# Performance work log

Measured on AMD Instinct MI355X. Metric: run time of the kernel, lower is better.

## Reference

```python
import jax, jax.numpy as jnp
import numpy as np

IN_CHANNELS = 192
KERNEL_SIZE = 3
GROUPS = 1
N_ITER = 3  # power_it_niter


def _gram_conv(K):
    """Gram step of the conv operator: G[a, b] = sum_o corr(K[o, a], K[o, b]).

    K: (co, ci, k, k) -> (ci, ci, 2k-1, 2k-1). This is the kernel of M^T M
    where M is the (zero-padded) conv operator with kernel K.
    """
    k = K.shape[-1]
    lhs = jnp.transpose(K, (1, 0, 2, 3))  # batch = a-index, channels = o
    rhs = jnp.transpose(K, (1, 0, 2, 3))  # out-chan = b-index, in-chan = o
    return jax.lax.conv_general_dilated(
        lhs, rhs, window_strides=(1, 1),
        padding=[(k - 1, k - 1), (k - 1, k - 1)],
        dimension_numbers=("NCHW", "OIHW", "NCHW"))


def _sigma_one_group(K, n_iter):
    """Gram-iteration spectral-norm estimate (Delattre et al. 2024).

    sigma(K_0) ~= prod_t f_t^(1/2^t) * ||K_T||_F^(1/2^T), f_t = Frobenius norm
    before each Gram squaring (normalization keeps values in fp range).
    """
    log_sigma = jnp.asarray(0.0, K.dtype)
    for t in range(n_iter):  # static unroll: kernel spatial size grows k -> 2k-1
        f = jnp.sqrt(jnp.sum(K * K))
        K = K / f
        log_sigma = log_sigma + jnp.log(f) / (2.0 ** t)
        K = _gram_conv(K)
    f_final = jnp.sqrt(jnp.sum(K * K))
    log_sigma = log_sigma + jnp.log(f_final) / (2.0 ** n_iter)
    return jnp.exp(log_sigma)


def compute_delattre2024(K, n_iter):
    # K: (groups, c, c, k, k) -> (groups,) per-group spectral norm estimates
    return jax.vmap(lambda g: _sigma_one_group(g, n_iter))(K)


def setup_inputs() -> dict:
    key = jax.random.key(0)
    kernel = jax.random.normal(
        key, (IN_CHANNELS * GROUPS, IN_CHANNELS, KERNEL_SIZE, KERNEL_SIZE),
        dtype=jnp.float32)
    return {"kernel": kernel}


def reference(kernel):
    g = GROUPS
    c = IN_CHANNELS // GROUPS
    K = kernel.reshape(g, c, c, KERNEL_SIZE, KERNEL_SIZE)
    sigmas = compute_delattre2024(K, N_ITER)  # (groups,)
    K = K / sigmas.reshape(-1, 1, 1, 1, 1)
    return K.reshape(IN_CHANNELS * GROUPS, IN_CHANNELS, KERNEL_SIZE, KERNEL_SIZE)
```

## Files before the change

### kernel.cpp

```cpp
#include <hip/hip_runtime.h>
#include <hip/hip_bf16.h>

typedef __bf16 bf16;
typedef __attribute__((ext_vector_type(8))) __bf16 bf16x8;
typedef __attribute__((ext_vector_type(4))) __bf16 bf16x4;
typedef __attribute__((ext_vector_type(4))) float f32x4;
typedef __attribute__((ext_vector_type(4))) int i32x4;
typedef __attribute__((ext_vector_type(2))) int i32x2;

#define CH 192
#define MAT (CH * CH)
#define NF 145
#define NELEM (CH * CH * 9)
#define XSCALE 9.765625e-4f
#define W17 0.36959913571644626f


__device__ __forceinline__ int swz8(int c, int r) {
    return (c & ~7) | ((c & 7) ^ (r & 7));
}

__global__ void k_tr(const float* __restrict__ K, float* __restrict__ Kt,
                     float* __restrict__ s3) {
    int p = blockIdx.x * 256 + threadIdx.x;
    if (p == 0) *s3 = 0.0f;
    int o = p / CH, a = p % CH;
    const float* src = K + (size_t)p * 9;
#pragma unroll
    for (int i = 0; i < 9; ++i)
        Kt[(size_t)i * MAT + a * CH + o] = src[i];
}

__global__ __launch_bounds__(1024, 4)
__attribute__((amdgpu_waves_per_eu(4, 4)))
void k_g3(const float* __restrict__ Kt, float* __restrict__ s3) {
    __shared__ __align__(16) bf16 lds[2 * MAT];
    __shared__ float twc[17], tws[17];
    __shared__ float red[16];
    int f = blockIdx.x;
    int tid = threadIdx.x;
    int lane = tid & 63, w = tid >> 6;
    int ml = lane & 15, kqc = lane >> 4;
    int rb = (w >> 2) * 48;
    int cb = (w & 3) * 48;

    if (tid < 17) {
        float s, c;
        __sincosf(-W17 * (float)tid, &s, &c);
        twc[tid] = c; tws[tid] = s;
    }
    __syncthreads();

    int fy, fx;
    if (f < 9) { fy = 0; fx = f; }
    else { int uu = f - 9; fy = 1 + uu / 17; fx = uu % 17; }
    float pyr = twc[fy], pyi = tws[fy];
    float pxr = twc[fx], pxi = tws[fx];
    int fx2 = 2 * fx; if (fx2 >= 17) fx2 -= 17;
    int fy2 = 2 * fy; if (fy2 >= 17) fy2 -= 17;
    float px2r = twc[fx2], px2i = tws[fx2];
    float py2r = twc[fy2], py2i = tws[fy2];
    float cR[9], cI[9];
    cR[0] = 1.0f;  cI[0] = 0.0f;
    cR[1] = pxr;   cI[1] = pxi;
    cR[2] = px2r;  cI[2] = px2i;
    cR[3] = pyr;   cI[3] = pyi;
    cR[4] = pyr * pxr - pyi * pxi;    cI[4] = pyr * pxi + pyi * pxr;
    cR[5] = pyr * px2r - pyi * px2i;  cI[5] = pyr * px2i + pyi * px2r;
    cR[6] = py2r;  cI[6] = py2i;
    cR[7] = py2r * pxr - py2i * pxi;  cI[7] = py2r * pxi + py2i * pxr;
    cR[8] = py2r * px2r - py2i * px2i; cI[8] = py2r * px2i + py2i * px2r;
#pragma unroll
    for (int i = 0; i < 9; ++i) { cR[i] *= XSCALE; cI[i] *= XSCALE; }

#pragma unroll 1
    for (int j5 = 0; j5 < 5; ++j5) {
        int cidx = j5 * 1024 + tid;
        if (cidx < 4608) {
            int a = cidx / 24, c = cidx % 24;
            const float* base = Kt + a * CH + c * 8;
            float xr0 = 0.f, xr1 = 0.f, xr2 = 0.f, xr3 = 0.f;
            float xr4 = 0.f, xr5 = 0.f, xr6 = 0.f, xr7 = 0.f;
            float xi0 = 0.f, xi1 = 0.f, xi2 = 0.f, xi3 = 0.f;
            float xi4 = 0.f, xi5 = 0.f, xi6 = 0.f, xi7 = 0.f;
#pragma unroll
            for (int i = 0; i < 9; ++i) {
                f32x4 lo = *(const f32x4*)(base + (size_t)i * MAT);
                f32x4 hi = *(const f32x4*)(base + (size_t)i * MAT + 4);
                float r = cR[i], m = cI[i];
                xr0 += r * lo[0]; xi0 += m * lo[0];
                xr1 += r * lo[1]; xi1 += m * lo[1];
                xr2 += r * lo[2]; xi2 += m * lo[2];
                xr3 += r * lo[3]; xi3 += m * lo[3];
                xr4 += r * hi[0]; xi4 += m * hi[0];
                xr5 += r * hi[1]; xi5 += m * hi[1];
                xr6 += r * hi[2]; xi6 += m * hi[2];
                xr7 += r * hi[3]; xi7 += m * hi[3];
            }
            bf16x8 vr, vi;
            vr[0] = (bf16)xr0; vr[1] = (bf16)xr1; vr[2] = (bf16)xr2; vr[3] = (bf16)xr3;
            vr[4] = (bf16)xr4; vr[5] = (bf16)xr5; vr[6] = (bf16)xr6; vr[7] = (bf16)xr7;
            vi[0] = (bf16)xi0; vi[1] = (bf16)xi1; vi[2] = (bf16)xi2; vi[3] = (bf16)xi3;
            vi[4] = (bf16)xi4; vi[5] = (bf16)xi5; vi[6] = (bf16)xi6; vi[7] = (bf16)xi7;
            int e = a * CH + swz8(c, a) * 8;
            *(i32x4*)&lds[e]       = __builtin_bit_cast(i32x4, vr);
            *(i32x4*)&lds[MAT + e] = __builtin_bit_cast(i32x4, vi);
        }
    }
    __syncthreads();

    int arow[3], abit[3], brow[3], bbit[3];
#pragma unroll
    for (int i = 0; i < 3; ++i) {
        int ra = rb + i * 16 + ml;
        arow[i] = ra * CH; abit[i] = ra & 7;
        int rc = cb + i * 16 + ml;
        brow[i] = rc * CH; bbit[i] = rc & 7;
    }

    f32x4 cr[3][3], ci[3][3];
#pragma unroll 1
    for (int round = 0; round < 3; ++round) {
        bool active = (round < 2) || (cb >= rb);
#pragma unroll
        for (int i = 0; i < 3; ++i)
#pragma unroll
            for (int j = 0; j < 3; ++j) {
                cr[i][j] = f32x4{0.f, 0.f, 0.f, 0.f};
                ci[i][j] = f32x4{0.f, 0.f, 0.f, 0.f};
            }
        if (active) {
#pragma unroll
            for (int ks8 = 0; ks8 < 24; ks8 += 4) {
                int c0 = ks8 + kqc;
                bf16x8 ar[3], ai[3];
#pragma unroll
                for (int mt = 0; mt < 3; ++mt) {
                    int e = arow[mt] + swz8(c0, abit[mt]) * 8;
                    ar[mt] = *(const bf16x8*)&lds[e];
                    ai[mt] = *(const bf16x8*)&lds[MAT + e];
                }
#pragma unroll
                for (int nt = 0; nt < 3; ++nt) {
                    int e = brow[nt] + swz8(c0, bbit[nt]) * 8;
                    bf16x8 br = *(const bf16x8*)&lds[e];
                    bf16x8 bi = *(const bf16x8*)&lds[MAT + e];
                    i32x4 u = __builtin_bit_cast(i32x4, br);
                    u ^= 0x80008000;
                    bf16x8 nbr = __builtin_bit_cast(bf16x8, u);
                    __builtin_amdgcn_s_setprio(1);
#pragma unroll
                    for (int mt = 0; mt < 3; ++mt) {
                        cr[mt][nt] = __builtin_amdgcn_mfma_f32_16x16x32_bf16(ar[mt], br,  cr[mt][nt], 0, 0, 0);
                        ci[mt][nt] = __builtin_amdgcn_mfma_f32_16x16x32_bf16(ar[mt], bi,  ci[mt][nt], 0, 0, 0);
                        cr[mt][nt] = __builtin_amdgcn_mfma_f32_16x16x32_bf16(ai[mt], bi,  cr[mt][nt], 0, 0, 0);
                        ci[mt][nt] = __builtin_amdgcn_mfma_f32_16x16x32_bf16(ai[mt], nbr, ci[mt][nt], 0, 0, 0);
                    }
                    __builtin_amdgcn_s_setprio(0);
                }
            }
        }
        if (round < 2) {
            __syncthreads();
            int lrq = kqc * 4;
#pragma unroll
            for (int mt = 0; mt < 3; ++mt) {
                int row0 = rb + mt * 16 + lrq;
                int rc = row0 >> 3, rlo = row0 & 7;
#pragma unroll
                for (int nt = 0; nt < 3; ++nt) {
                    int col = cb + nt * 16 + ml;
                    int e = col * CH + swz8(rc, col) * 8 + rlo;
                    bf16x4 pr, pi;
#pragma unroll
                    for (int rr = 0; rr < 4; ++rr) {
                        pr[rr] = (bf16)cr[mt][nt][rr];
                        pi[rr] = (bf16)ci[mt][nt][rr];
                    }
                    *(i32x2*)&lds[e]       = __builtin_bit_cast(i32x2, pr);
                    *(i32x2*)&lds[MAT + e] = __builtin_bit_cast(i32x2, pi);
                }
            }
            __syncthreads();
        }
    }

    float loc = 0.f;
#pragma unroll
    for (int mt = 0; mt < 3; ++mt)
#pragma unroll
        for (int nt = 0; nt < 3; ++nt)
#pragma unroll
            for (int rr = 0; rr < 4; ++rr)
                loc += cr[mt][nt][rr] * cr[mt][nt][rr] + ci[mt][nt][rr] * ci[mt][nt][rr];
    float wt = (cb > rb) ? 2.0f : ((cb == rb) ? 1.0f : 0.0f);
    loc *= wt;
#pragma unroll
    for (int off = 32; off > 0; off >>= 1) loc += __shfl_down(loc, off, 64);
    if (lane == 0) red[w] = loc;
    __syncthreads();
    if (tid == 0) {
        float base = (f == 0) ? 1.0f : 2.0f;
        float acc = 0.f;
#pragma unroll
        for (int i = 0; i < 16; ++i) acc += red[i];
        atomicAdd(s3, base * acc);
    }
}

__global__ void k_scale(const float* __restrict__ K, float* __restrict__ out,
                        const float* __restrict__ s3) {
    float sig = 1024.0f * exp2f(log2f((*s3) * (1.0f / 289.0f)) * 0.0625f);
    float inv = 1.0f / sig;
    int i = (blockIdx.x * 256 + threadIdx.x) * 4;
    f32x4 v = *(const f32x4*)(K + i);
    v *= inv;
    *(f32x4*)(out + i) = v;
}

extern "C" void kernel_launch(void* const* d_in, const int* in_sizes, int n_in,
                              void* d_out, int out_size, void* d_ws, size_t ws_size,
                              hipStream_t stream) {
    const float* K = (const float*)d_in[0];
    float* out = (float*)d_out;
    char* ws = (char*)d_ws;
    float* s3 = (float*)ws;
    float* Kt = (float*)(ws + 256);

    k_tr<<<NELEM / (256 * 9), 256, 0, stream>>>(K, Kt, s3);
    k_g3<<<NF, 1024, 0, stream>>>(Kt, s3);
    k_scale<<<NELEM / 1024, 256, 0, stream>>>(K, out, s3);
}
```

Before: 108.2 us.

## Halve block to 512 threads with 96x48 warp tiles in Gram kernel

The Gram-matrix kernel now runs 8 waves per block instead of 16, and each wave computes a 96x48 output tile (6x3 MFMA subtiles) instead of 48x48. This reuses each B-fragment load across twice as many MFMAs and cuts LDS read traffic per flop. The swizzle index is simplified to depend only on lane bits, and the final-round triangle skip becomes per-element weighting at a coarser tile granularity. In exchange, register pressure is higher, fewer waves are available to hide latency, and the last round does more redundant work on diagonal tiles.

```diff
diff --git a/kernel.cpp b/kernel.cpp
--- a/kernel.cpp
+++ b/kernel.cpp
@@ -31,18 +31,20 @@
         Kt[(size_t)i * MAT + a * CH + o] = src[i];
 }
 
-__global__ __launch_bounds__(1024, 4)
-__attribute__((amdgpu_waves_per_eu(4, 4)))
+__global__ __launch_bounds__(512, 2)
+__attribute__((amdgpu_waves_per_eu(2, 2)))
 void k_g3(const float* __restrict__ Kt, float* __restrict__ s3) {
     __shared__ __align__(16) bf16 lds[2 * MAT];
     __shared__ float twc[17], tws[17];
-    __shared__ float red[16];
+    __shared__ float red[8];
     int f = blockIdx.x;
     int tid = threadIdx.x;
     int lane = tid & 63, w = tid >> 6;
     int ml = lane & 15, kqc = lane >> 4;
-    int rb = (w >> 2) * 48;
+    int mlb = ml & 7;
+    int rb = (w >> 2) * 96;
     int cb = (w & 3) * 48;
+    bool comp3 = !(rb == 96 && cb < 96);
 
     if (tid < 17) {
         float s, c;
@@ -74,56 +76,51 @@
     for (int i = 0; i < 9; ++i) { cR[i] *= XSCALE; cI[i] *= XSCALE; }
 
 #pragma unroll 1
-    for (int j5 = 0; j5 < 5; ++j5) {
-        int cidx = j5 * 1024 + tid;
-        if (cidx < 4608) {
-            int a = cidx / 24, c = cidx % 24;
-            const float* base = Kt + a * CH + c * 8;
-            float xr0 = 0.f, xr1 = 0.f, xr2 = 0.f, xr3 = 0.f;
-            float xr4 = 0.f, xr5 = 0.f, xr6 = 0.f, xr7 = 0.f;
-            float xi0 = 0.f, xi1 = 0.f, xi2 = 0.f, xi3 = 0.f;
-            float xi4 = 0.f, xi5 = 0.f, xi6 = 0.f, xi7 = 0.f;
-#pragma unroll
-            for (int i = 0; i < 9; ++i) {
-                f32x4 lo = *(const f32x4*)(base + (size_t)i * MAT);
-                f32x4 hi = *(const f32x4*)(base + (size_t)i * MAT + 4);
-                float r = cR[i], m = cI[i];
-                xr0 += r * lo[0]; xi0 += m * lo[0];
-                xr1 += r * lo[1]; xi1 += m * lo[1];
-                xr2 += r * lo[2]; xi2 += m * lo[2];
-                xr3 += r * lo[3]; xi3 += m * lo[3];
-                xr4 += r * hi[0]; xi4 += m * hi[0];
-                xr5 += r * hi[1]; xi5 += m * hi[1];
-                xr6 += r * hi[2]; xi6 += m * hi[2];
-                xr7 += r * hi[3]; xi7 += m * hi[3];
-            }
-            bf16x8 vr, vi;
-            vr[0] = (bf16)xr0; vr[1] = (bf16)xr1; vr[2] = (bf16)xr2; vr[3] = (bf16)xr3;
-            vr[4] = (bf16)xr4; vr[5] = (bf16)xr5; vr[6] = (bf16)xr6; vr[7] = (bf16)xr7;
-            vi[0] = (bf16)xi0; vi[1] = (bf16)xi1; vi[2] = (bf16)xi2; vi[3] = (bf16)xi3;
-            vi[4] = (bf16)xi4; vi[5] = (bf16)xi5; vi[6] = (bf16)xi6; vi[7] = (bf16)xi7;
-            int e = a * CH + swz8(c, a) * 8;
-            *(i32x4*)&lds[e]       = __builtin_bit_cast(i32x4, vr);
-            *(i32x4*)&lds[MAT + e] = __builtin_bit_cast(i32x4, vi);
+    for (int j = 0; j < 9; ++j) {
+        int cidx = j * 512 + tid;
+        int a = cidx / 24, c = cidx % 24;
+        const float* base = Kt + a * CH + c * 8;
+        float xr0 = 0.f, xr1 = 0.f, xr2 = 0.f, xr3 = 0.f;
+        float xr4 = 0.f, xr5 = 0.f, xr6 = 0.f, xr7 = 0.f;
+        float xi0 = 0.f, xi1 = 0.f, xi2 = 0.f, xi3 = 0.f;
+        float xi4 = 0.f, xi5 = 0.f, xi6 = 0.f, xi7 = 0.f;
+#pragma unroll
+        for (int i = 0; i < 9; ++i) {
+            f32x4 lo = *(const f32x4*)(base + (size_t)i * MAT);
+            f32x4 hi = *(const f32x4*)(base + (size_t)i * MAT + 4);
+            float r = cR[i], m = cI[i];
+            xr0 += r * lo[0]; xi0 += m * lo[0];
+            xr1 += r * lo[1]; xi1 += m * lo[1];
+            xr2 += r * lo[2]; xi2 += m * lo[2];
+            xr3 += r * lo[3]; xi3 += m * lo[3];
+            xr4 += r * hi[0]; xi4 += m * hi[0];
+            xr5 += r * hi[1]; xi5 += m * hi[1];
+            xr6 += r * hi[2]; xi6 += m * hi[2];
+            xr7 += r * hi[3]; xi7 += m * hi[3];
         }
+        bf16x8 vr, vi;
+        vr[0] = (bf16)xr0; vr[1] = (bf16)xr1; vr[2] = (bf16)xr2; vr[3] = (bf16)xr3;
+        vr[4] = (bf16)xr4; vr[5] = (bf16)xr5; vr[6] = (bf16)xr6; vr[7] = (bf16)xr7;
+        vi[0] = (bf16)xi0; vi[1] = (bf16)xi1; vi[2] = (bf16)xi2; vi[3] = (bf16)xi3;
+        vi[4] = (bf16)xi4; vi[5] = (bf16)xi5; vi[6] = (bf16)xi6; vi[7] = (bf16)xi7;
+        int e = a * CH + swz8(c, a) * 8;
+        *(i32x4*)&lds[e]       = __builtin_bit_cast(i32x4, vr);
+        *(i32x4*)&lds[MAT + e] = __builtin_bit_cast(i32x4, vi);
     }
     __syncthreads();
 
-    int arow[3], abit[3], brow[3], bbit[3];
-#pragma unroll
-    for (int i = 0; i < 3; ++i) {
-        int ra = rb + i * 16 + ml;
-        arow[i] = ra * CH; abit[i] = ra & 7;
-        int rc = cb + i * 16 + ml;
-        brow[i] = rc * CH; bbit[i] = rc & 7;
-    }
-
-    f32x4 cr[3][3], ci[3][3];
+    int arow[6], brow[3];
+#pragma unroll
+    for (int i = 0; i < 6; ++i) arow[i] = (rb + i * 16 + ml) * CH;
+#pragma unroll
+    for (int i = 0; i < 3; ++i) brow[i] = (cb + i * 16 + ml) * CH;
+
+    f32x4 cr[6][3], ci[6][3];
 #pragma unroll 1
     for (int round = 0; round < 3; ++round) {
-        bool active = (round < 2) || (cb >= rb);
-#pragma unroll
-        for (int i = 0; i < 3; ++i)
+        bool active = (round < 2) || comp3;
+#pragma unroll
+        for (int i = 0; i < 6; ++i)
 #pragma unroll
             for (int j = 0; j < 3; ++j) {
                 cr[i][j] = f32x4{0.f, 0.f, 0.f, 0.f};
@@ -132,17 +129,17 @@
         if (active) {
 #pragma unroll
             for (int ks8 = 0; ks8 < 24; ks8 += 4) {
-                int c0 = ks8 + kqc;
-                bf16x8 ar[3], ai[3];
-#pragma unroll
-                for (int mt = 0; mt < 3; ++mt) {
-                    int e = arow[mt] + swz8(c0, abit[mt]) * 8;
+                int sw = swz8(ks8 + kqc, mlb) * 8;
+                bf16x8 ar[6], ai[6];
+#pragma unroll
+                for (int mt = 0; mt < 6; ++mt) {
+                    int e = arow[mt] + sw;
                     ar[mt] = *(const bf16x8*)&lds[e];
                     ai[mt] = *(const bf16x8*)&lds[MAT + e];
                 }
 #pragma unroll
                 for (int nt = 0; nt < 3; ++nt) {
-                    int e = brow[nt] + swz8(c0, bbit[nt]) * 8;
+                    int e = brow[nt] + sw;
                     bf16x8 br = *(const bf16x8*)&lds[e];
                     bf16x8 bi = *(const bf16x8*)&lds[MAT + e];
                     i32x4 u = __builtin_bit_cast(i32x4, br);
@@ -150,12 +147,17 @@
                     bf16x8 nbr = __builtin_bit_cast(bf16x8, u);
                     __builtin_amdgcn_s_setprio(1);
 #pragma unroll
-                    for (int mt = 0; mt < 3; ++mt) {
+                    for (int mt = 0; mt < 6; ++mt)
                         cr[mt][nt] = __builtin_amdgcn_mfma_f32_16x16x32_bf16(ar[mt], br,  cr[mt][nt], 0, 0, 0);
+#pragma unroll
+                    for (int mt = 0; mt < 6; ++mt)
                         ci[mt][nt] = __builtin_amdgcn_mfma_f32_16x16x32_bf16(ar[mt], bi,  ci[mt][nt], 0, 0, 0);
+#pragma unroll
+                    for (int mt = 0; mt < 6; ++mt)
                         cr[mt][nt] = __builtin_amdgcn_mfma_f32_16x16x32_bf16(ai[mt], bi,  cr[mt][nt], 0, 0, 0);
+#pragma unroll
+                    for (int mt = 0; mt < 6; ++mt)
                         ci[mt][nt] = __builtin_amdgcn_mfma_f32_16x16x32_bf16(ai[mt], nbr, ci[mt][nt], 0, 0, 0);
-                    }
                     __builtin_amdgcn_s_setprio(0);
                 }
             }
@@ -164,13 +166,13 @@
             __syncthreads();
             int lrq = kqc * 4;
 #pragma unroll
-            for (int mt = 0; mt < 3; ++mt) {
+            for (int mt = 0; mt < 6; ++mt) {
                 int row0 = rb + mt * 16 + lrq;
                 int rc = row0 >> 3, rlo = row0 & 7;
 #pragma unroll
                 for (int nt = 0; nt < 3; ++nt) {
                     int col = cb + nt * 16 + ml;
-                    int e = col * CH + swz8(rc, col) * 8 + rlo;
+                    int e = col * CH + swz8(rc, mlb) * 8 + rlo;
                     bf16x4 pr, pi;
 #pragma unroll
                     for (int rr = 0; rr < 4; ++rr) {
@@ -187,14 +189,17 @@
 
     float loc = 0.f;
 #pragma unroll
-    for (int mt = 0; mt < 3; ++mt)
+    for (int mt = 0; mt < 6; ++mt)
 #pragma unroll
         for (int nt = 0; nt < 3; ++nt)
 #pragma unroll
-            for (int rr = 0; rr < 4; ++rr)
-                loc += cr[mt][nt][rr] * cr[mt][nt][rr] + ci[mt][nt][rr] * ci[mt][nt][rr];
-    float wt = (cb > rb) ? 2.0f : ((cb == rb) ? 1.0f : 0.0f);
-    loc *= wt;
+            for (int rr = 0; rr < 4; ++rr) {
+                int row = rb + mt * 16 + kqc * 4 + rr;
+                int col = cb + nt * 16 + ml;
+                float wt = (col > row) ? 2.0f : ((col == row) ? 1.0f : 0.0f);
+                loc += wt * (cr[mt][nt][rr] * cr[mt][nt][rr] +
+                             ci[mt][nt][rr] * ci[mt][nt][rr]);
+            }
 #pragma unroll
     for (int off = 32; off > 0; off >>= 1) loc += __shfl_down(loc, off, 64);
     if (lane == 0) red[w] = loc;
@@ -203,7 +208,7 @@
         float base = (f == 0) ? 1.0f : 2.0f;
         float acc = 0.f;
 #pragma unroll
-        for (int i = 0; i < 16; ++i) acc += red[i];
+        for (int i = 0; i < 8; ++i) acc += red[i];
         atomicAdd(s3, base * acc);
     }
 }
@@ -228,6 +233,6 @@
     float* Kt = (float*)(ws + 256);
 
     k_tr<<<NELEM / (256 * 9), 256, 0, stream>>>(K, Kt, s3);
-    k_g3<<<NF, 1024, 0, stream>>>(Kt, s3);
+    k_g3<<<NF, 512, 0, stream>>>(Kt, s3);
     k_scale<<<NELEM / 1024, 256, 0, stream>>>(K, out, s3);
 }
```

New measurement: 104.1 us. 1.04x faster.
